# Kernel tuning notes

Hardware: AMD Instinct MI355X
Metric: run time of the kernel (lower is better)

Reference implementation:

```python
import jax, jax.numpy as jnp
import numpy as np

N = 50000      # nodes
E = 800000     # edges (avg degree 16)
D = 64         # input_dim
L = 64         # latent_dim


def setup_inputs() -> dict:
    key = jax.random.key(0)
    k1, k2, k3, k4, k5, k6 = jax.random.split(key, 6)
    x = jax.random.normal(k1, (N, D), dtype=jnp.float32)
    weight = jax.random.normal(k2, (D, L), dtype=jnp.float32) / np.sqrt(D)
    bias = jax.random.normal(k3, (L,), dtype=jnp.float32) * 0.01
    # strictly positive degrees to keep division well-behaved
    node_degree = jax.random.uniform(k4, (N, 1), dtype=jnp.float32) + 1.0
    edge_src = jax.random.randint(k5, (E,), 0, N, dtype=jnp.int32)
    edge_dst = jax.random.randint(k6, (E,), 0, N, dtype=jnp.int32)
    return {"x": x, "weight": weight, "bias": bias,
            "node_degree": node_degree,
            "edge_src": edge_src, "edge_dst": edge_dst}


def reference(x, weight, bias, node_degree, edge_src, edge_dst):
    # gnn_spmm(adj, x): sparse aggregate over incoming edges -> [N, D]
    agg = jax.ops.segment_sum(x[edge_src], edge_dst, num_segments=N)
    pooled = agg + x                      # residual self-connection
    node_linear = pooled @ weight + bias  # dense projection [N, L]
    normalized = node_linear / node_degree  # normalize_embedding == 2
    return jax.nn.relu(normalized)
```

## Files before the change

kernel.cpp:

```cpp
#include <hip/hip_runtime.h>
#include <hip/hip_fp16.h>

#define N_NODES 50000
#define DIM 64
#define CB 391
#define CAP 2560
#define EB 6400
#define SCAP 1408
#define PLW 68

typedef _Float16 half8 __attribute__((ext_vector_type(8)));
typedef _Float16 half4v __attribute__((ext_vector_type(4)));
typedef float floatx4 __attribute__((ext_vector_type(4)));

#define WS_CURSOR  0
#define WS_COARSE  2048
#define WS_XH      (WS_COARSE + 4003840)
#define WS_WT      (WS_XH + 6400000)

__global__ void __launch_bounds__(256) prep_kernel(
        const float* __restrict__ x, const float* __restrict__ W,
        const int* __restrict__ edge_src, const int* __restrict__ edge_dst,
        int* __restrict__ cursor, unsigned int* __restrict__ coarse,
        _Float16* __restrict__ xh, _Float16* __restrict__ wt,
        int E, int pa) {
    int b = blockIdx.x, t = threadIdx.x;
    if (b < pa) {
        __shared__ int lhist[CB];
        __shared__ int lbase[CB];
        for (int i = t; i < CB; i += 256) lhist[i] = 0;
        __syncthreads();

        int base = b * EB;
        int end = base + EB; if (end > E) end = E;

        for (int i = base + t; i < end; i += 256) {
            atomicAdd(&lhist[edge_dst[i] >> 7], 1);
        }
        __syncthreads();
        for (int i = t; i < CB; i += 256) {
            lbase[i] = atomicAdd(&cursor[i], lhist[i]);
            lhist[i] = 0;
        }
        __syncthreads();
        for (int i = base + t; i < end; i += 256) {
            int s = edge_src[i];
            int d = edge_dst[i];
            int bk = d >> 7;
            int r = atomicAdd(&lhist[bk], 1);
            coarse[(size_t)bk * CAP + lbase[bk] + r] =
                ((unsigned int)s << 7) | (unsigned int)(d & 127);
        }
    } else if (b < pa + 3125) {
        int i = (b - pa) * 256 + t;
        float4 v = reinterpret_cast<const float4*>(x)[i];
        half4v h = { (_Float16)v.x, (_Float16)v.y, (_Float16)v.z, (_Float16)v.w };
        reinterpret_cast<half4v*>(xh)[i] = h;
    } else {
        #pragma unroll
        for (int i = 0; i < 16; ++i) {
            int idx = t * 16 + i;
            int n = idx >> 6, k = idx & 63;
            wt[idx] = (_Float16)W[k * DIM + n];
        }
    }
}

__global__ void __launch_bounds__(256) fused_kernel(
        const _Float16* __restrict__ xh,
        const _Float16* __restrict__ wt,
        const float* __restrict__ bias,
        const float* __restrict__ deg,
        const int* __restrict__ cursor,
        const unsigned int* __restrict__ coarse,
        float* __restrict__ out) {
    __shared__ unsigned int sedges[SCAP];
    __shared__ float pl[64 * PLW];
    __shared__ int hist[64];
    __shared__ int excl[64];
    __shared__ int cur[64];

    int t = threadIdx.x;
    int b = blockIdx.x;
    int bucket = (b >> 4) * 8 + (b & 7);
    int half = (b >> 3) & 1;
    if (bucket >= CB) return;
    int nb = bucket * 128 + half * 64;
    int cnt = cursor[bucket];
    const unsigned int* cbk = coarse + (size_t)bucket * CAP;

    if (t < 64) hist[t] = 0;
    __syncthreads();
    for (int i = t; i < cnt; i += 256) {
        unsigned int e = cbk[i];
        int loc = (int)(e & 127u);
        if ((loc >> 6) == half) atomicAdd(&hist[loc & 63], 1);
    }
    __syncthreads();

    if (t < 64) {
        int v = hist[t];
        int s = v;
        #pragma unroll
        for (int off = 1; off < 64; off <<= 1) {
            int u = __shfl_up(s, off);
            if (t >= off) s += u;
        }
        excl[t] = s - v;
        cur[t]  = s - v;
    }
    __syncthreads();

    for (int i = t; i < cnt; i += 256) {
        unsigned int e = cbk[i];
        int loc = (int)(e & 127u);
        if ((loc >> 6) == half) {
            int p = atomicAdd(&cur[loc & 63], 1);
            sedges[p] = e >> 7;
        }
    }
    __syncthreads();

    int g = t >> 3;
    int c = t & 7;
    #pragma unroll
    for (int pass = 0; pass < 2; ++pass) {
        int loc = g + pass * 32;
        int node = nb + loc;
        float acc[8];
        #pragma unroll
        for (int j = 0; j < 8; ++j) acc[j] = 0.f;
        int off = excl[loc];
        int ct = (node < N_NODES) ? hist[loc] : 0;
        int k = 0;
        for (; k + 8 <= ct; k += 8) {
            int sid[8];
            #pragma unroll
            for (int u = 0; u < 8; ++u) sid[u] = (int)sedges[off + k + u];
            half8 v[8];
            #pragma unroll
            for (int u = 0; u < 8; ++u)
                v[u] = *reinterpret_cast<const half8*>(xh + (size_t)sid[u] * DIM + c * 8);
            #pragma unroll
            for (int u = 0; u < 8; ++u) {
                #pragma unroll
                for (int j = 0; j < 8; ++j) acc[j] += (float)v[u][j];
            }
        }
        for (; k + 4 <= ct; k += 4) {
            int sid[4];
            #pragma unroll
            for (int u = 0; u < 4; ++u) sid[u] = (int)sedges[off + k + u];
            half8 v[4];
            #pragma unroll
            for (int u = 0; u < 4; ++u)
                v[u] = *reinterpret_cast<const half8*>(xh + (size_t)sid[u] * DIM + c * 8);
            #pragma unroll
            for (int u = 0; u < 4; ++u) {
                #pragma unroll
                for (int j = 0; j < 8; ++j) acc[j] += (float)v[u][j];
            }
        }
        for (; k < ct; ++k) {
            int s0 = (int)sedges[off + k];
            half8 v0 = *reinterpret_cast<const half8*>(xh + (size_t)s0 * DIM + c * 8);
            #pragma unroll
            for (int j = 0; j < 8; ++j) acc[j] += (float)v0[j];
        }
        if (node < N_NODES) {
            half8 r = *reinterpret_cast<const half8*>(
                xh + (size_t)node * DIM + c * 8);
            float* p = &pl[loc * PLW + c * 8];
            #pragma unroll
            for (int j = 0; j < 8; ++j) p[j] = acc[j] + (float)r[j];
        }
    }
    __syncthreads();

    int wv = t >> 6;
    int lane = t & 63;
    int m = lane & 15;
    int q = lane >> 4;
    int lbase = wv * 16;

    const float* ap = &pl[(lbase + m) * PLW];
    half8 a0, a1;
    #pragma unroll
    for (int j = 0; j < 8; ++j) a0[j] = (_Float16)ap[q * 8 + j];
    #pragma unroll
    for (int j = 0; j < 8; ++j) a1[j] = (_Float16)ap[32 + q * 8 + j];

    floatx4 acc4[4];
    #pragma unroll
    for (int tt = 0; tt < 4; ++tt) {
        half8 b0 = *reinterpret_cast<const half8*>(wt + (size_t)(tt * 16 + m) * DIM + q * 8);
        half8 b1 = *reinterpret_cast<const half8*>(wt + (size_t)(tt * 16 + m) * DIM + q * 8 + 32);
        floatx4 cfrag = {0.f, 0.f, 0.f, 0.f};
        cfrag = __builtin_amdgcn_mfma_f32_16x16x32_f16(a0, b0, cfrag, 0, 0, 0);
        cfrag = __builtin_amdgcn_mfma_f32_16x16x32_f16(a1, b1, cfrag, 0, 0, 0);
        acc4[tt] = cfrag;
    }

    #pragma unroll
    for (int r = 0; r < 4; ++r) {
        int row = q * 4 + r;
        int node = nb + lbase + row;
        if (node < N_NODES) {
            float inv = 1.0f / deg[node];
            #pragma unroll
            for (int tt = 0; tt < 4; ++tt) {
                float v = (acc4[tt][r] + bias[tt * 16 + m]) * inv;
                out[(size_t)node * DIM + tt * 16 + m] = fmaxf(v, 0.f);
            }
        }
    }
}

extern "C" void kernel_launch(void* const* d_in, const int* in_sizes, int n_in,
                              void* d_out, int out_size, void* d_ws, size_t ws_size,
                              hipStream_t stream) {
    const float* x        = (const float*)d_in[0];
    const float* weight   = (const float*)d_in[1];
    const float* bias     = (const float*)d_in[2];
    const float* node_deg = (const float*)d_in[3];
    const int*   edge_src = (const int*)d_in[4];
    const int*   edge_dst = (const int*)d_in[5];
    float* out = (float*)d_out;
    const int E = in_sizes[4];

    char* ws = (char*)d_ws;
    int*          cursor = (int*)(ws + WS_CURSOR);
    unsigned int* coarse = (unsigned int*)(ws + WS_COARSE);
    _Float16*     xh     = (_Float16*)(ws + WS_XH);
    _Float16*     wt     = (_Float16*)(ws + WS_WT);

    hipMemsetAsync(cursor, 0, CB * sizeof(int), stream);

    int pa = (E + EB - 1) / EB;
    prep_kernel<<<pa + 3125 + 1, 256, 0, stream>>>(
        x, weight, edge_src, edge_dst, cursor, coarse, xh, wt, E, pa);

    fused_kernel<<<784, 256, 0, stream>>>(
        xh, wt, bias, node_deg, cursor, coarse, out);
}
```

Baseline: 120.0 us.

## Replace per-node histogram+scan with fixed-capacity bins; keep edges in registers during prep

The fused kernel drops its counting pass and prefix scan. Each node's incoming source ids now go straight into a fixed 64-slot shared-memory bin via an atomic cursor, which removes one full read of the bucket's coarse edge list and two barriers. The prep kernel moves to 512 threads with 12 edges per thread held in registers, so edge_src and edge_dst are read once instead of twice, and the conversion and weight blocks are resized to match. The fixed bin capacity assumes no node has more than 64 incoming edges in a half-bucket. A heavier-tailed degree distribution would overflow a bin, and the larger shared-memory footprint could lower occupancy.

```diff
diff --git a/kernel.cpp b/kernel.cpp
--- a/kernel.cpp
+++ b/kernel.cpp
@@ -5,8 +5,9 @@
 #define DIM 64
 #define CB 391
 #define CAP 2560
-#define EB 6400
-#define SCAP 1408
+#define EPT 12
+#define EB (512 * EPT)
+#define BINCAP 64
 #define PLW 68
 
 typedef _Float16 half8 __attribute__((ext_vector_type(8)));
@@ -18,7 +19,7 @@
 #define WS_XH      (WS_COARSE + 4003840)
 #define WS_WT      (WS_XH + 6400000)
 
-__global__ void __launch_bounds__(256) prep_kernel(
+__global__ void __launch_bounds__(512) prep_kernel(
         const float* __restrict__ x, const float* __restrict__ W,
         const int* __restrict__ edge_src, const int* __restrict__ edge_dst,
         int* __restrict__ cursor, unsigned int* __restrict__ coarse,
@@ -28,38 +29,48 @@
     if (b < pa) {
         __shared__ int lhist[CB];
         __shared__ int lbase[CB];
-        for (int i = t; i < CB; i += 256) lhist[i] = 0;
+        for (int i = t; i < CB; i += 512) lhist[i] = 0;
         __syncthreads();
 
         int base = b * EB;
-        int end = base + EB; if (end > E) end = E;
-
-        for (int i = base + t; i < end; i += 256) {
-            atomicAdd(&lhist[edge_dst[i] >> 7], 1);
+        unsigned int pk[EPT];
+        int bk[EPT];
+        #pragma unroll
+        for (int j = 0; j < EPT; ++j) {
+            int e = base + j * 512 + t;
+            bk[j] = -1;
+            if (e < E) {
+                int s = edge_src[e];
+                int d = edge_dst[e];
+                bk[j] = d >> 7;
+                pk[j] = ((unsigned int)s << 7) | (unsigned int)(d & 127);
+                atomicAdd(&lhist[bk[j]], 1);
+            }
         }
         __syncthreads();
-        for (int i = t; i < CB; i += 256) {
+        for (int i = t; i < CB; i += 512) {
             lbase[i] = atomicAdd(&cursor[i], lhist[i]);
             lhist[i] = 0;
         }
         __syncthreads();
-        for (int i = base + t; i < end; i += 256) {
-            int s = edge_src[i];
-            int d = edge_dst[i];
-            int bk = d >> 7;
-            int r = atomicAdd(&lhist[bk], 1);
-            coarse[(size_t)bk * CAP + lbase[bk] + r] =
-                ((unsigned int)s << 7) | (unsigned int)(d & 127);
-        }
-    } else if (b < pa + 3125) {
-        int i = (b - pa) * 256 + t;
-        float4 v = reinterpret_cast<const float4*>(x)[i];
-        half4v h = { (_Float16)v.x, (_Float16)v.y, (_Float16)v.z, (_Float16)v.w };
-        reinterpret_cast<half4v*>(xh)[i] = h;
+        #pragma unroll
+        for (int j = 0; j < EPT; ++j) {
+            if (bk[j] >= 0) {
+                int r = atomicAdd(&lhist[bk[j]], 1);
+                coarse[(size_t)bk[j] * CAP + lbase[bk[j]] + r] = pk[j];
+            }
+        }
+    } else if (b < pa + 1563) {
+        int i = (b - pa) * 512 + t;
+        if (i < N_NODES * DIM / 4) {
+            float4 v = reinterpret_cast<const float4*>(x)[i];
+            half4v h = { (_Float16)v.x, (_Float16)v.y, (_Float16)v.z, (_Float16)v.w };
+            reinterpret_cast<half4v*>(xh)[i] = h;
+        }
     } else {
         #pragma unroll
-        for (int i = 0; i < 16; ++i) {
-            int idx = t * 16 + i;
+        for (int i = 0; i < 8; ++i) {
+            int idx = t * 8 + i;
             int n = idx >> 6, k = idx & 63;
             wt[idx] = (_Float16)W[k * DIM + n];
         }
@@ -74,10 +85,8 @@
         const int* __restrict__ cursor,
         const unsigned int* __restrict__ coarse,
         float* __restrict__ out) {
-    __shared__ unsigned int sedges[SCAP];
+    __shared__ int sedges[64 * BINCAP];
     __shared__ float pl[64 * PLW];
-    __shared__ int hist[64];
-    __shared__ int excl[64];
     __shared__ int cur[64];
 
     int t = threadIdx.x;
@@ -89,34 +98,16 @@
     int cnt = cursor[bucket];
     const unsigned int* cbk = coarse + (size_t)bucket * CAP;
 
-    if (t < 64) hist[t] = 0;
-    __syncthreads();
-    for (int i = t; i < cnt; i += 256) {
-        unsigned int e = cbk[i];
-        int loc = (int)(e & 127u);
-        if ((loc >> 6) == half) atomicAdd(&hist[loc & 63], 1);
-    }
-    __syncthreads();
-
-    if (t < 64) {
-        int v = hist[t];
-        int s = v;
-        #pragma unroll
-        for (int off = 1; off < 64; off <<= 1) {
-            int u = __shfl_up(s, off);
-            if (t >= off) s += u;
-        }
-        excl[t] = s - v;
-        cur[t]  = s - v;
-    }
+    if (t < 64) cur[t] = 0;
     __syncthreads();
 
     for (int i = t; i < cnt; i += 256) {
         unsigned int e = cbk[i];
         int loc = (int)(e & 127u);
         if ((loc >> 6) == half) {
-            int p = atomicAdd(&cur[loc & 63], 1);
-            sedges[p] = e >> 7;
+            int bin = loc & 63;
+            int p = atomicAdd(&cur[bin], 1);
+            sedges[bin * BINCAP + p] = (int)(e >> 7);
         }
     }
     __syncthreads();
@@ -130,13 +121,13 @@
         float acc[8];
         #pragma unroll
         for (int j = 0; j < 8; ++j) acc[j] = 0.f;
-        int off = excl[loc];
-        int ct = (node < N_NODES) ? hist[loc] : 0;
+        const int* bp = &sedges[loc * BINCAP];
+        int ct = cur[loc];
         int k = 0;
         for (; k + 8 <= ct; k += 8) {
             int sid[8];
             #pragma unroll
-            for (int u = 0; u < 8; ++u) sid[u] = (int)sedges[off + k + u];
+            for (int u = 0; u < 8; ++u) sid[u] = bp[k + u];
             half8 v[8];
             #pragma unroll
             for (int u = 0; u < 8; ++u)
@@ -150,7 +141,7 @@
         for (; k + 4 <= ct; k += 4) {
             int sid[4];
             #pragma unroll
-            for (int u = 0; u < 4; ++u) sid[u] = (int)sedges[off + k + u];
+            for (int u = 0; u < 4; ++u) sid[u] = bp[k + u];
             half8 v[4];
             #pragma unroll
             for (int u = 0; u < 4; ++u)
@@ -162,7 +153,7 @@
             }
         }
         for (; k < ct; ++k) {
-            int s0 = (int)sedges[off + k];
+            int s0 = bp[k];
             half8 v0 = *reinterpret_cast<const half8*>(xh + (size_t)s0 * DIM + c * 8);
             #pragma unroll
             for (int j = 0; j < 8; ++j) acc[j] += (float)v0[j];
@@ -237,7 +228,7 @@
     hipMemsetAsync(cursor, 0, CB * sizeof(int), stream);
 
     int pa = (E + EB - 1) / EB;
-    prep_kernel<<<pa + 3125 + 1, 256, 0, stream>>>(
+    prep_kernel<<<pa + 1563 + 1, 512, 0, stream>>>(
         x, weight, edge_src, edge_dst, cursor, coarse, xh, wt, E, pa);
 
     fused_kernel<<<784, 256, 0, stream>>>(
```

Result: faster. 113.0 us (median of 2 runs) (-5.8%).
